# Kernel tuning notes

Hardware: AMD Instinct MI355X
Metric: run time of the kernel (lower is better)

## Reference

```python
import jax, jax.numpy as jnp
import numpy as np

B, C, P, N = 16, 512, 4, 1024


def setup_inputs() -> dict:
    key = jax.random.key(0)
    k1, k2, k3, k4, k5 = jax.random.split(key, 5)
    s = 1.0 / np.sqrt(C)
    return {
        "x": jax.random.normal(k1, (B, C, P, N), dtype=jnp.float32),
        "w_qkv": jax.random.normal(k2, (1 + 2 * C, C), dtype=jnp.float32) * s,
        "b_qkv": jax.random.normal(k3, (1 + 2 * C,), dtype=jnp.float32) * 0.01,
        "w_out": jax.random.normal(k4, (C, C), dtype=jnp.float32) * s,
        "b_out": jax.random.normal(k5, (C,), dtype=jnp.float32) * 0.01,
    }


def reference(x, w_qkv, b_qkv, w_out, b_out):
    # 1x1 conv == channel GEMM: [B,C,P,N] x [O,C] -> [B,O,P,N]
    qkv = jnp.einsum('bcpn,oc->bopn', x, w_qkv) + b_qkv[None, :, None, None]
    query = qkv[:, :1]            # [B,1,P,N]
    key_t = qkv[:, 1:1 + C]       # [B,C,P,N]
    value = qkv[:, 1 + C:]        # [B,C,P,N]
    # softmax over token axis N (attn_drop is identity at inference)
    context_scores = jax.nn.softmax(query, axis=-1)           # [B,1,P,N]
    # broadcast mul + reduce over N (fused; no explicit expand)
    context_vector = jnp.sum(key_t * context_scores, axis=-1, keepdims=True)  # [B,C,P,1]
    out = jax.nn.relu(value) * context_vector                 # [B,C,P,N]
    out = jnp.einsum('bcpn,oc->bopn', out, w_out) + b_out[None, :, None, None]
    return out
```

## Files before the change

### kernel.cpp

```cpp
#include <hip/hip_runtime.h>
#include <math.h>

#define BB 16
#define C  512
#define P  4
#define NN 1024
#define BP (BB*P)
#define PN (P*NN)

typedef short bf16x8 __attribute__((ext_vector_type(8)));
typedef float f32x4  __attribute__((ext_vector_type(4)));

__device__ __forceinline__ unsigned short bf16rne(float f) {
    unsigned u = __float_as_uint(f);
    u += 0x7FFFu + ((u >> 16) & 1u);
    return (unsigned short)(u >> 16);
}
__device__ __forceinline__ float bf16tof(unsigned short h) {
    return __uint_as_float(((unsigned)h) << 16);
}

__global__ __launch_bounds__(256) void k_split(const float* __restrict__ w_qkv,
                                               const float* __restrict__ w_out,
                                               unsigned short* __restrict__ wv_hi,
                                               unsigned short* __restrict__ wv_lo,
                                               unsigned short* __restrict__ wo_hi,
                                               unsigned short* __restrict__ wo_lo) {
    const int i = blockIdx.x * 256 + threadIdx.x;
    const int e = i * 4;
    const float* src; unsigned short *dh, *dl; int off;
    if (e < C * C) { src = w_qkv + (size_t)(1 + C) * C; dh = wv_hi; dl = wv_lo; off = e; }
    else           { src = w_out;                       dh = wo_hi; dl = wo_lo; off = e - C * C; }
    const float4 v = *reinterpret_cast<const float4*>(src + off);
    const float vv[4] = {v.x, v.y, v.z, v.w};
    unsigned short h[4], l[4];
    #pragma unroll
    for (int j = 0; j < 4; ++j) {
        h[j] = bf16rne(vv[j]);
        l[j] = bf16rne(vv[j] - bf16tof(h[j]));
    }
    uint2 ph, pl;
    ph.x = (unsigned)h[0] | ((unsigned)h[1] << 16);
    ph.y = (unsigned)h[2] | ((unsigned)h[3] << 16);
    pl.x = (unsigned)l[0] | ((unsigned)l[1] << 16);
    pl.y = (unsigned)l[2] | ((unsigned)l[3] << 16);
    *reinterpret_cast<uint2*>(dh + off) = ph;
    *reinterpret_cast<uint2*>(dl + off) = pl;
}

__global__ __launch_bounds__(256) void k_query(const float* __restrict__ x,
                                               const float* __restrict__ w_qkv,
                                               const float* __restrict__ b_qkv,
                                               float* __restrict__ query) {
    __shared__ float wq[C];
    const int bp  = blockIdx.x >> 2;
    const int q4  = blockIdx.x & 3;
    const int b   = bp >> 2, p = bp & 3;
    const int tid = threadIdx.x;
    for (int i = tid; i < C; i += 256) wq[i] = w_qkv[i];
    __syncthreads();
    const int n = q4 * 256 + tid;
    const float* xb = x + (size_t)b * C * PN + (size_t)p * NN + n;
    float a0 = 0.f, a1 = 0.f, a2 = 0.f, a3 = 0.f;
    #pragma unroll 4
    for (int c = 0; c < C; c += 4) {
        a0 = fmaf(xb[(size_t)(c + 0) * PN], wq[c + 0], a0);
        a1 = fmaf(xb[(size_t)(c + 1) * PN], wq[c + 1], a1);
        a2 = fmaf(xb[(size_t)(c + 2) * PN], wq[c + 2], a2);
        a3 = fmaf(xb[(size_t)(c + 3) * PN], wq[c + 3], a3);
    }
    query[bp * NN + n] = b_qkv[0] + ((a0 + a1) + (a2 + a3));
}

__global__ __launch_bounds__(256) void k_softmax(const float* __restrict__ query,
                                                 float* __restrict__ scores) {
    __shared__ float red[256];
    const int bp = blockIdx.x, tid = threadIdx.x;
    const float* q = query + bp * NN;
    float v[4];
    float m = -INFINITY;
    #pragma unroll
    for (int j = 0; j < 4; ++j) { v[j] = q[tid + 256 * j]; m = fmaxf(m, v[j]); }
    red[tid] = m; __syncthreads();
    for (int s = 128; s > 0; s >>= 1) {
        if (tid < s) red[tid] = fmaxf(red[tid], red[tid + s]);
        __syncthreads();
    }
    m = red[0]; __syncthreads();
    float sum = 0.f;
    #pragma unroll
    for (int j = 0; j < 4; ++j) { v[j] = expf(v[j] - m); sum += v[j]; }
    red[tid] = sum; __syncthreads();
    for (int s = 128; s > 0; s >>= 1) {
        if (tid < s) red[tid] += red[tid + s];
        __syncthreads();
    }
    const float inv = 1.0f / red[0];
    #pragma unroll
    for (int j = 0; j < 4; ++j) scores[bp * NN + tid + 256 * j] = v[j] * inv;
}

__global__ __launch_bounds__(256) void k_xs(const float* __restrict__ x,
                                            const float* __restrict__ scores,
                                            float* __restrict__ xs) {
    __shared__ float sc[NN];
    const int bp = blockIdx.x >> 3, cc = blockIdx.x & 7;
    const int b = bp >> 2, p = bp & 3;
    const int tid = threadIdx.x;
    for (int i = tid; i < NN; i += 256) sc[i] = scores[bp * NN + i];
    __syncthreads();
    const int wave = tid >> 6, lane = tid & 63;
    const float* xb = x + (size_t)b * C * PN + (size_t)p * NN;
    for (int k = 0; k < 16; ++k) {
        const int c = cc * 64 + wave * 16 + k;
        const float* row = xb + (size_t)c * PN;
        float acc = 0.f;
        #pragma unroll
        for (int j = 0; j < 16; ++j) acc = fmaf(row[lane + 64 * j], sc[lane + 64 * j], acc);
        #pragma unroll
        for (int off = 32; off > 0; off >>= 1) acc += __shfl_down(acc, off);
        if (lane == 0) xs[bp * C + c] = acc;
    }
}

__global__ __launch_bounds__(256) void k_cv(const float* __restrict__ xs,
                                            const float* __restrict__ w_qkv,
                                            const float* __restrict__ b_qkv,
                                            float* __restrict__ cv) {
    __shared__ float xsl[C];
    const int bp = blockIdx.x, tid = threadIdx.x;
    for (int i = tid; i < C; i += 256) xsl[i] = xs[bp * C + i];
    __syncthreads();
    const int wave = tid >> 6, lane = tid & 63;
    for (int o = wave; o < C; o += 4) {
        const float* wr = w_qkv + (size_t)(1 + o) * C;
        float acc = 0.f;
        #pragma unroll
        for (int j = 0; j < 8; ++j) acc = fmaf(wr[lane + 64 * j], xsl[lane + 64 * j], acc);
        #pragma unroll
        for (int off = 32; off > 0; off >>= 1) acc += __shfl_down(acc, off);
        if (lane == 0) cv[bp * C + o] = acc + b_qkv[1 + o];
    }
}

#define ALD 520
#define XLD 40
#define SLD 68

__global__ __launch_bounds__(512, 1) void k_vo(
    const float* __restrict__ x,
    const unsigned short* __restrict__ wv_hi, const unsigned short* __restrict__ wv_lo,
    const unsigned short* __restrict__ wo_hi, const unsigned short* __restrict__ wo_lo,
    const float* __restrict__ b_qkv, const float* __restrict__ b_out,
    const float* __restrict__ cv, float* __restrict__ out) {

    extern __shared__ char lds_raw[];
    unsigned short* act_hi = (unsigned short*)lds_raw;
    unsigned short* act_lo = act_hi + 64 * ALD;
    unsigned short* xt_hi  = act_lo + 64 * ALD;
    unsigned short* xt_lo  = xt_hi + 64 * XLD;
    float*          scratch = (float*)(xt_lo + 64 * XLD);

    const int nt = blockIdx.x, bp = blockIdx.y;
    const int b = bp >> 2, p = bp & 3;
    const int n0 = nt * 64;
    const int tid = threadIdx.x;
    const int w  = tid >> 6;
    const int l  = tid & 63;
    const int lr = l & 15;
    const int lg = l >> 4;

    const float* xb = x + (size_t)b * C * PN + (size_t)p * NN + n0;

    const int s_kk = tid >> 4, s_n4 = (tid & 15) * 4;
    const int g_col = tid & 63, g_k4 = (tid >> 6) * 4;

    f32x4 acc[4][4];
    #pragma unroll
    for (int m = 0; m < 4; ++m)
        #pragma unroll
        for (int n = 0; n < 4; ++n) acc[m][n] = (f32x4){0.f, 0.f, 0.f, 0.f};

    for (int kt = 0; kt < 16; ++kt) {
        *reinterpret_cast<float4*>(&scratch[s_kk * SLD + s_n4]) =
            *reinterpret_cast<const float4*>(xb + (size_t)(kt * 32 + s_kk) * PN + s_n4);
        __syncthreads();
        {
            unsigned short h[4], lo[4];
            #pragma unroll
            for (int j = 0; j < 4; ++j) {
                const float v = scratch[(g_k4 + j) * SLD + g_col];
                h[j]  = bf16rne(v);
                lo[j] = bf16rne(v - bf16tof(h[j]));
            }
            uint2 ph, pl;
            ph.x = (unsigned)h[0]  | ((unsigned)h[1]  << 16);
            ph.y = (unsigned)h[2]  | ((unsigned)h[3]  << 16);
            pl.x = (unsigned)lo[0] | ((unsigned)lo[1] << 16);
            pl.y = (unsigned)lo[2] | ((unsigned)lo[3] << 16);
            *reinterpret_cast<uint2*>(&xt_hi[g_col * XLD + g_k4]) = ph;
            *reinterpret_cast<uint2*>(&xt_lo[g_col * XLD + g_k4]) = pl;
        }
        __syncthreads();
        bf16x8 bh[4], bl[4];
        #pragma unroll
        for (int n = 0; n < 4; ++n) {
            bh[n] = *reinterpret_cast<const bf16x8*>(&xt_hi[(n * 16 + lr) * XLD + lg * 8]);
            bl[n] = *reinterpret_cast<const bf16x8*>(&xt_lo[(n * 16 + lr) * XLD + lg * 8]);
        }
        #pragma unroll
        for (int m = 0; m < 4; ++m) {
            const int row = w * 64 + m * 16 + lr;
            const bf16x8 ah = *reinterpret_cast<const bf16x8*>(&wv_hi[(size_t)row * C + kt * 32 + lg * 8]);
            const bf16x8 al = *reinterpret_cast<const bf16x8*>(&wv_lo[(size_t)row * C + kt * 32 + lg * 8]);
            #pragma unroll
            for (int n = 0; n < 4; ++n) {
                acc[m][n] = __builtin_amdgcn_mfma_f32_16x16x32_bf16(ah, bh[n], acc[m][n], 0, 0, 0);
                acc[m][n] = __builtin_amdgcn_mfma_f32_16x16x32_bf16(ah, bl[n], acc[m][n], 0, 0, 0);
                acc[m][n] = __builtin_amdgcn_mfma_f32_16x16x32_bf16(al, bh[n], acc[m][n], 0, 0, 0);
            }
        }
    }

    {
        const float* bq  = b_qkv + 1 + C;
        const float* cvb = cv + bp * C;
        #pragma unroll
        for (int m = 0; m < 4; ++m) {
            const int r0 = w * 64 + m * 16 + lg * 4;
            float bias[4], cvv[4];
            #pragma unroll
            for (int j = 0; j < 4; ++j) { bias[j] = bq[r0 + j]; cvv[j] = cvb[r0 + j]; }
            #pragma unroll
            for (int n = 0; n < 4; ++n) {
                unsigned short hh[4], ll[4];
                #pragma unroll
                for (int j = 0; j < 4; ++j) {
                    const float av = fmaxf(acc[m][n][j] + bias[j], 0.f) * cvv[j];
                    hh[j] = bf16rne(av);
                    ll[j] = bf16rne(av - bf16tof(hh[j]));
                }
                uint2 ph, pl;
                ph.x = (unsigned)hh[0] | ((unsigned)hh[1] << 16);
                ph.y = (unsigned)hh[2] | ((unsigned)hh[3] << 16);
                pl.x = (unsigned)ll[0] | ((unsigned)ll[1] << 16);
                pl.y = (unsigned)ll[2] | ((unsigned)ll[3] << 16);
                *reinterpret_cast<uint2*>(&act_hi[(n * 16 + lr) * ALD + r0]) = ph;
                *reinterpret_cast<uint2*>(&act_lo[(n * 16 + lr) * ALD + r0]) = pl;
            }
        }
    }
    __syncthreads();

    f32x4 acc2[4][4];
    #pragma unroll
    for (int m = 0; m < 4; ++m)
        #pragma unroll
        for (int n = 0; n < 4; ++n) acc2[m][n] = (f32x4){0.f, 0.f, 0.f, 0.f};

    for (int kt = 0; kt < 16; ++kt) {
        bf16x8 bh[4], bl[4];
        #pragma unroll
        for (int n = 0; n < 4; ++n) {
            bh[n] = *reinterpret_cast<const bf16x8*>(&act_hi[(n * 16 + lr) * ALD + kt * 32 + lg * 8]);
            bl[n] = *reinterpret_cast<const bf16x8*>(&act_lo[(n * 16 + lr) * ALD + kt * 32 + lg * 8]);
        }
        #pragma unroll
        for (int m = 0; m < 4; ++m) {
            const int row = w * 64 + m * 16 + lr;
            const bf16x8 ah = *reinterpret_cast<const bf16x8*>(&wo_hi[(size_t)row * C + kt * 32 + lg * 8]);
            const bf16x8 al = *reinterpret_cast<const bf16x8*>(&wo_lo[(size_t)row * C + kt * 32 + lg * 8]);
            #pragma unroll
            for (int n = 0; n < 4; ++n) {
                acc2[m][n] = __builtin_amdgcn_mfma_f32_16x16x32_bf16(ah, bh[n], acc2[m][n], 0, 0, 0);
                acc2[m][n] = __builtin_amdgcn_mfma_f32_16x16x32_bf16(ah, bl[n], acc2[m][n], 0, 0, 0);
                acc2[m][n] = __builtin_amdgcn_mfma_f32_16x16x32_bf16(al, bh[n], acc2[m][n], 0, 0, 0);
            }
        }
    }

    #pragma unroll
    for (int m = 0; m < 4; ++m) {
        #pragma unroll
        for (int j = 0; j < 4; ++j) {
            const int row = w * 64 + m * 16 + lg * 4 + j;
            const float bo = b_out[row];
            float* orow = out + ((size_t)(b * C + row) * P + p) * NN + n0;
            #pragma unroll
            for (int n = 0; n < 4; ++n)
                orow[n * 16 + lr] = acc2[m][n][j] + bo;
        }
    }
}

extern "C" void kernel_launch(void* const* d_in, const int* in_sizes, int n_in,
                              void* d_out, int out_size, void* d_ws, size_t ws_size,
                              hipStream_t stream) {
    const float* x     = (const float*)d_in[0];
    const float* w_qkv = (const float*)d_in[1];
    const float* b_qkv = (const float*)d_in[2];
    const float* w_out = (const float*)d_in[3];
    const float* b_out = (const float*)d_in[4];
    float* out = (float*)d_out;

    float* query  = (float*)d_ws;
    float* scores = query + BP * NN;
    float* xs     = scores + BP * NN;
    float* cv     = xs + BP * C;
    unsigned short* wsp = (unsigned short*)(cv + BP * C);
    unsigned short* wv_hi = wsp;
    unsigned short* wv_lo = wsp + C * C;
    unsigned short* wo_hi = wsp + 2 * C * C;
    unsigned short* wo_lo = wsp + 3 * C * C;

    k_split  <<<dim3(512),    256, 0, stream>>>(w_qkv, w_out, wv_hi, wv_lo, wo_hi, wo_lo);
    k_query  <<<dim3(BP * 4), 256, 0, stream>>>(x, w_qkv, b_qkv, query);
    k_softmax<<<dim3(BP),     256, 0, stream>>>(query, scores);
    k_xs     <<<dim3(BP * 8), 256, 0, stream>>>(x, scores, xs);
    k_cv     <<<dim3(BP),     256, 0, stream>>>(xs, w_qkv, b_qkv, cv);

    const size_t ldsbytes = (size_t)(2 * 64 * ALD + 2 * 64 * XLD) * 2 + (size_t)(32 * SLD) * 4;
    k_vo<<<dim3(16, BP), 512, ldsbytes, stream>>>(x, wv_hi, wv_lo, wo_hi, wo_lo,
                                                  b_qkv, b_out, cv, out);
}
```

Measured before the change: 649.1 us.

## Double-buffer x tiles in k_vo with fragment-ordered LDS, and vectorize the reductions

k_vo now prefetches the next x k-slice into registers while MFMAs run on the current one. It converts the slice straight into a double-buffered LDS layout that matches the MFMA fragment order, which removes the fp32 scratch transpose and one barrier per iteration. The intermediate activation is also stored in fragment order, so it can be read back with contiguous 16-byte loads. k_query is split over channel chunks with float4 loads, writing partial sums that k_softmax adds up. The bias is dropped there, which is valid because softmax is shift-invariant. k_xs uses float4 loads across more blocks. The trade-offs are an extra partial-sum buffer and higher register pressure from the prefetch.

```diff
diff --git a/kernel.cpp b/kernel.cpp
--- a/kernel.cpp
+++ b/kernel.cpp
@@ -10,30 +10,31 @@
 
 typedef short bf16x8 __attribute__((ext_vector_type(8)));
 typedef float f32x4  __attribute__((ext_vector_type(4)));
-
-__device__ __forceinline__ unsigned short bf16rne(float f) {
+typedef unsigned short ushort_t;
+
+__device__ __forceinline__ ushort_t bf16rne(float f) {
     unsigned u = __float_as_uint(f);
     u += 0x7FFFu + ((u >> 16) & 1u);
-    return (unsigned short)(u >> 16);
-}
-__device__ __forceinline__ float bf16tof(unsigned short h) {
+    return (ushort_t)(u >> 16);
+}
+__device__ __forceinline__ float bf16tof(ushort_t h) {
     return __uint_as_float(((unsigned)h) << 16);
 }
 
 __global__ __launch_bounds__(256) void k_split(const float* __restrict__ w_qkv,
                                                const float* __restrict__ w_out,
-                                               unsigned short* __restrict__ wv_hi,
-                                               unsigned short* __restrict__ wv_lo,
-                                               unsigned short* __restrict__ wo_hi,
-                                               unsigned short* __restrict__ wo_lo) {
+                                               ushort_t* __restrict__ wv_hi,
+                                               ushort_t* __restrict__ wv_lo,
+                                               ushort_t* __restrict__ wo_hi,
+                                               ushort_t* __restrict__ wo_lo) {
     const int i = blockIdx.x * 256 + threadIdx.x;
     const int e = i * 4;
-    const float* src; unsigned short *dh, *dl; int off;
+    const float* src; ushort_t *dh, *dl; int off;
     if (e < C * C) { src = w_qkv + (size_t)(1 + C) * C; dh = wv_hi; dl = wv_lo; off = e; }
     else           { src = w_out;                       dh = wo_hi; dl = wo_lo; off = e - C * C; }
     const float4 v = *reinterpret_cast<const float4*>(src + off);
     const float vv[4] = {v.x, v.y, v.z, v.w};
-    unsigned short h[4], l[4];
+    ushort_t h[4], l[4];
     #pragma unroll
     for (int j = 0; j < 4; ++j) {
         h[j] = bf16rne(vv[j]);
@@ -50,37 +51,42 @@
 
 __global__ __launch_bounds__(256) void k_query(const float* __restrict__ x,
                                                const float* __restrict__ w_qkv,
-                                               const float* __restrict__ b_qkv,
-                                               float* __restrict__ query) {
-    __shared__ float wq[C];
-    const int bp  = blockIdx.x >> 2;
-    const int q4  = blockIdx.x & 3;
-    const int b   = bp >> 2, p = bp & 3;
+                                               float4* __restrict__ qpart4) {
+    __shared__ float wq[64];
+    const int bp = blockIdx.x >> 3, cc = blockIdx.x & 7;
+    const int b = bp >> 2, p = bp & 3;
     const int tid = threadIdx.x;
-    for (int i = tid; i < C; i += 256) wq[i] = w_qkv[i];
-    __syncthreads();
-    const int n = q4 * 256 + tid;
-    const float* xb = x + (size_t)b * C * PN + (size_t)p * NN + n;
-    float a0 = 0.f, a1 = 0.f, a2 = 0.f, a3 = 0.f;
-    #pragma unroll 4
-    for (int c = 0; c < C; c += 4) {
-        a0 = fmaf(xb[(size_t)(c + 0) * PN], wq[c + 0], a0);
-        a1 = fmaf(xb[(size_t)(c + 1) * PN], wq[c + 1], a1);
-        a2 = fmaf(xb[(size_t)(c + 2) * PN], wq[c + 2], a2);
-        a3 = fmaf(xb[(size_t)(c + 3) * PN], wq[c + 3], a3);
-    }
-    query[bp * NN + n] = b_qkv[0] + ((a0 + a1) + (a2 + a3));
-}
-
-__global__ __launch_bounds__(256) void k_softmax(const float* __restrict__ query,
-                                                 float* __restrict__ scores) {
+    if (tid < 64) wq[tid] = w_qkv[cc * 64 + tid];
+    __syncthreads();
+    const float* xb = x + (size_t)b * C * PN + (size_t)p * NN;
+    f32x4 acc[8];
+    #pragma unroll
+    for (int a = 0; a < 8; ++a) acc[a] = (f32x4){0.f, 0.f, 0.f, 0.f};
+    #pragma unroll 8
+    for (int i = 0; i < 64; ++i) {
+        const float4 v = *reinterpret_cast<const float4*>(xb + (size_t)(cc * 64 + i) * PN + tid * 4);
+        const float wv = wq[i];
+        acc[i & 7][0] = fmaf(v.x, wv, acc[i & 7][0]);
+        acc[i & 7][1] = fmaf(v.y, wv, acc[i & 7][1]);
+        acc[i & 7][2] = fmaf(v.z, wv, acc[i & 7][2]);
+        acc[i & 7][3] = fmaf(v.w, wv, acc[i & 7][3]);
+    }
+    f32x4 s = ((acc[0] + acc[1]) + (acc[2] + acc[3])) + ((acc[4] + acc[5]) + (acc[6] + acc[7]));
+    float4 o; o.x = s[0]; o.y = s[1]; o.z = s[2]; o.w = s[3];
+    qpart4[(cc * BP + bp) * 256 + tid] = o;
+}
+
+__global__ __launch_bounds__(256) void k_softmax(const float4* __restrict__ qpart4,
+                                                 float4* __restrict__ scores4) {
     __shared__ float red[256];
     const int bp = blockIdx.x, tid = threadIdx.x;
-    const float* q = query + bp * NN;
-    float v[4];
-    float m = -INFINITY;
-    #pragma unroll
-    for (int j = 0; j < 4; ++j) { v[j] = q[tid + 256 * j]; m = fmaxf(m, v[j]); }
+    float v[4] = {0.f, 0.f, 0.f, 0.f};
+    #pragma unroll
+    for (int cc = 0; cc < 8; ++cc) {
+        const float4 q = qpart4[(cc * BP + bp) * 256 + tid];
+        v[0] += q.x; v[1] += q.y; v[2] += q.z; v[3] += q.w;
+    }
+    float m = fmaxf(fmaxf(v[0], v[1]), fmaxf(v[2], v[3]));
     red[tid] = m; __syncthreads();
     for (int s = 128; s > 0; s >>= 1) {
         if (tid < s) red[tid] = fmaxf(red[tid], red[tid + s]);
@@ -96,27 +102,36 @@
         __syncthreads();
     }
     const float inv = 1.0f / red[0];
-    #pragma unroll
-    for (int j = 0; j < 4; ++j) scores[bp * NN + tid + 256 * j] = v[j] * inv;
+    float4 o; o.x = v[0] * inv; o.y = v[1] * inv; o.z = v[2] * inv; o.w = v[3] * inv;
+    scores4[bp * 256 + tid] = o;
 }
 
 __global__ __launch_bounds__(256) void k_xs(const float* __restrict__ x,
-                                            const float* __restrict__ scores,
+                                            const float4* __restrict__ scores4,
                                             float* __restrict__ xs) {
-    __shared__ float sc[NN];
-    const int bp = blockIdx.x >> 3, cc = blockIdx.x & 7;
+    __shared__ float4 sc4[256];
+    const int bp = blockIdx.x >> 4, cc = blockIdx.x & 15;
     const int b = bp >> 2, p = bp & 3;
     const int tid = threadIdx.x;
-    for (int i = tid; i < NN; i += 256) sc[i] = scores[bp * NN + i];
+    sc4[tid] = scores4[bp * 256 + tid];
     __syncthreads();
     const int wave = tid >> 6, lane = tid & 63;
     const float* xb = x + (size_t)b * C * PN + (size_t)p * NN;
-    for (int k = 0; k < 16; ++k) {
-        const int c = cc * 64 + wave * 16 + k;
-        const float* row = xb + (size_t)c * PN;
-        float acc = 0.f;
-        #pragma unroll
-        for (int j = 0; j < 16; ++j) acc = fmaf(row[lane + 64 * j], sc[lane + 64 * j], acc);
+    #pragma unroll
+    for (int r = 0; r < 8; ++r) {
+        const int c = cc * 32 + wave * 8 + r;
+        const float4* row4 = reinterpret_cast<const float4*>(xb + (size_t)c * PN);
+        float a0 = 0.f, a1 = 0.f, a2 = 0.f, a3 = 0.f;
+        #pragma unroll
+        for (int j = 0; j < 4; ++j) {
+            const float4 xv = row4[lane + 64 * j];
+            const float4 sv = sc4[lane + 64 * j];
+            a0 = fmaf(xv.x, sv.x, a0);
+            a1 = fmaf(xv.y, sv.y, a1);
+            a2 = fmaf(xv.z, sv.z, a2);
+            a3 = fmaf(xv.w, sv.w, a3);
+        }
+        float acc = (a0 + a1) + (a2 + a3);
         #pragma unroll
         for (int off = 32; off > 0; off >>= 1) acc += __shfl_down(acc, off);
         if (lane == 0) xs[bp * C + c] = acc;
@@ -143,23 +158,19 @@
     }
 }
 
-#define ALD 520
-#define XLD 40
-#define SLD 68
+#define XTFH 2048
 
 __global__ __launch_bounds__(512, 1) void k_vo(
     const float* __restrict__ x,
-    const unsigned short* __restrict__ wv_hi, const unsigned short* __restrict__ wv_lo,
-    const unsigned short* __restrict__ wo_hi, const unsigned short* __restrict__ wo_lo,
+    const ushort_t* __restrict__ wv_hi, const ushort_t* __restrict__ wv_lo,
+    const ushort_t* __restrict__ wo_hi, const ushort_t* __restrict__ wo_lo,
     const float* __restrict__ b_qkv, const float* __restrict__ b_out,
     const float* __restrict__ cv, float* __restrict__ out) {
 
     extern __shared__ char lds_raw[];
-    unsigned short* act_hi = (unsigned short*)lds_raw;
-    unsigned short* act_lo = act_hi + 64 * ALD;
-    unsigned short* xt_hi  = act_lo + 64 * ALD;
-    unsigned short* xt_lo  = xt_hi + 64 * XLD;
-    float*          scratch = (float*)(xt_lo + 64 * XLD);
+    ushort_t* actf_hi = (ushort_t*)lds_raw;
+    ushort_t* actf_lo = actf_hi + 16 * 4 * 64 * 8;
+    ushort_t* xtf     = actf_lo + 16 * 4 * 64 * 8;
 
     const int nt = blockIdx.x, bp = blockIdx.y;
     const int b = bp >> 2, p = bp & 3;
@@ -172,8 +183,9 @@
 
     const float* xb = x + (size_t)b * C * PN + (size_t)p * NN + n0;
 
-    const int s_kk = tid >> 4, s_n4 = (tid & 15) * 4;
-    const int g_col = tid & 63, g_k4 = (tid >> 6) * 4;
+    const int g_col = tid & 63;
+    const int g_k4  = (tid >> 6) * 4;
+    const int st_off = (((g_col >> 4) * 64 + (g_k4 >> 3) * 16 + (g_col & 15)) * 8) + (g_k4 & 7);
 
     f32x4 acc[4][4];
     #pragma unroll
@@ -181,45 +193,71 @@
         #pragma unroll
         for (int n = 0; n < 4; ++n) acc[m][n] = (f32x4){0.f, 0.f, 0.f, 0.f};
 
+    {
+        float xg[4];
+        #pragma unroll
+        for (int jj = 0; jj < 4; ++jj) xg[jj] = xb[(size_t)(g_k4 + jj) * PN + g_col];
+        ushort_t h[4], lo[4];
+        #pragma unroll
+        for (int jj = 0; jj < 4; ++jj) {
+            h[jj]  = bf16rne(xg[jj]);
+            lo[jj] = bf16rne(xg[jj] - bf16tof(h[jj]));
+        }
+        uint2 ph, pl;
+        ph.x = (unsigned)h[0]  | ((unsigned)h[1]  << 16);
+        ph.y = (unsigned)h[2]  | ((unsigned)h[3]  << 16);
+        pl.x = (unsigned)lo[0] | ((unsigned)lo[1] << 16);
+        pl.y = (unsigned)lo[2] | ((unsigned)lo[3] << 16);
+        *reinterpret_cast<uint2*>(&xtf[st_off])        = ph;
+        *reinterpret_cast<uint2*>(&xtf[XTFH + st_off]) = pl;
+    }
+    __syncthreads();
+
     for (int kt = 0; kt < 16; ++kt) {
-        *reinterpret_cast<float4*>(&scratch[s_kk * SLD + s_n4]) =
-            *reinterpret_cast<const float4*>(xb + (size_t)(kt * 32 + s_kk) * PN + s_n4);
-        __syncthreads();
-        {
-            unsigned short h[4], lo[4];
-            #pragma unroll
-            for (int j = 0; j < 4; ++j) {
-                const float v = scratch[(g_k4 + j) * SLD + g_col];
-                h[j]  = bf16rne(v);
-                lo[j] = bf16rne(v - bf16tof(h[j]));
+        const int cur = kt & 1;
+        float xg[4];
+        if (kt < 15) {
+            #pragma unroll
+            for (int jj = 0; jj < 4; ++jj)
+                xg[jj] = xb[(size_t)((kt + 1) * 32 + g_k4 + jj) * PN + g_col];
+        }
+        const ushort_t* xh = xtf + cur * 2 * XTFH;
+        const ushort_t* xl = xh + XTFH;
+        bf16x8 bh[4], bl[4];
+        #pragma unroll
+        for (int n = 0; n < 4; ++n) {
+            bh[n] = *reinterpret_cast<const bf16x8*>(&xh[(n * 64 + l) * 8]);
+            bl[n] = *reinterpret_cast<const bf16x8*>(&xl[(n * 64 + l) * 8]);
+        }
+        #pragma unroll
+        for (int m = 0; m < 4; ++m) {
+            const int row = w * 64 + m * 16 + lr;
+            const bf16x8 ah = *reinterpret_cast<const bf16x8*>(&wv_hi[(size_t)row * C + kt * 32 + lg * 8]);
+            const bf16x8 al = *reinterpret_cast<const bf16x8*>(&wv_lo[(size_t)row * C + kt * 32 + lg * 8]);
+            #pragma unroll
+            for (int n = 0; n < 4; ++n) {
+                acc[m][n] = __builtin_amdgcn_mfma_f32_16x16x32_bf16(ah, bh[n], acc[m][n], 0, 0, 0);
+                acc[m][n] = __builtin_amdgcn_mfma_f32_16x16x32_bf16(ah, bl[n], acc[m][n], 0, 0, 0);
+                acc[m][n] = __builtin_amdgcn_mfma_f32_16x16x32_bf16(al, bh[n], acc[m][n], 0, 0, 0);
+            }
+        }
+        if (kt < 15) {
+            ushort_t* dh = xtf + (cur ^ 1) * 2 * XTFH;
+            ushort_t h[4], lo[4];
+            #pragma unroll
+            for (int jj = 0; jj < 4; ++jj) {
+                h[jj]  = bf16rne(xg[jj]);
+                lo[jj] = bf16rne(xg[jj] - bf16tof(h[jj]));
             }
             uint2 ph, pl;
             ph.x = (unsigned)h[0]  | ((unsigned)h[1]  << 16);
             ph.y = (unsigned)h[2]  | ((unsigned)h[3]  << 16);
             pl.x = (unsigned)lo[0] | ((unsigned)lo[1] << 16);
             pl.y = (unsigned)lo[2] | ((unsigned)lo[3] << 16);
-            *reinterpret_cast<uint2*>(&xt_hi[g_col * XLD + g_k4]) = ph;
-            *reinterpret_cast<uint2*>(&xt_lo[g_col * XLD + g_k4]) = pl;
+            *reinterpret_cast<uint2*>(&dh[st_off])        = ph;
+            *reinterpret_cast<uint2*>(&dh[XTFH + st_off]) = pl;
         }
         __syncthreads();
-        bf16x8 bh[4], bl[4];
-        #pragma unroll
-        for (int n = 0; n < 4; ++n) {
-            bh[n] = *reinterpret_cast<const bf16x8*>(&xt_hi[(n * 16 + lr) * XLD + lg * 8]);
-            bl[n] = *reinterpret_cast<const bf16x8*>(&xt_lo[(n * 16 + lr) * XLD + lg * 8]);
-        }
-        #pragma unroll
-        for (int m = 0; m < 4; ++m) {
-            const int row = w * 64 + m * 16 + lr;
-            const bf16x8 ah = *reinterpret_cast<const bf16x8*>(&wv_hi[(size_t)row * C + kt * 32 + lg * 8]);
-            const bf16x8 al = *reinterpret_cast<const bf16x8*>(&wv_lo[(size_t)row * C + kt * 32 + lg * 8]);
-            #pragma unroll
-            for (int n = 0; n < 4; ++n) {
-                acc[m][n] = __builtin_amdgcn_mfma_f32_16x16x32_bf16(ah, bh[n], acc[m][n], 0, 0, 0);
-                acc[m][n] = __builtin_amdgcn_mfma_f32_16x16x32_bf16(ah, bl[n], acc[m][n], 0, 0, 0);
-                acc[m][n] = __builtin_amdgcn_mfma_f32_16x16x32_bf16(al, bh[n], acc[m][n], 0, 0, 0);
-            }
-        }
     }
 
     {
@@ -227,13 +265,16 @@
         const float* cvb = cv + bp * C;
         #pragma unroll
         for (int m = 0; m < 4; ++m) {
-            const int r0 = w * 64 + m * 16 + lg * 4;
+            const int rbase = w * 64 + m * 16 + lg * 4;
+            const int ktp = w * 2 + (m >> 1);
+            const int lgp = (m * 2 + (lg >> 1)) & 3;
+            const int j0p = (lg & 1) * 4;
             float bias[4], cvv[4];
             #pragma unroll
-            for (int j = 0; j < 4; ++j) { bias[j] = bq[r0 + j]; cvv[j] = cvb[r0 + j]; }
+            for (int j = 0; j < 4; ++j) { bias[j] = bq[rbase + j]; cvv[j] = cvb[rbase + j]; }
             #pragma unroll
             for (int n = 0; n < 4; ++n) {
-                unsigned short hh[4], ll[4];
+                ushort_t hh[4], ll[4];
                 #pragma unroll
                 for (int j = 0; j < 4; ++j) {
                     const float av = fmaxf(acc[m][n][j] + bias[j], 0.f) * cvv[j];
@@ -245,8 +286,9 @@
                 ph.y = (unsigned)hh[2] | ((unsigned)hh[3] << 16);
                 pl.x = (unsigned)ll[0] | ((unsigned)ll[1] << 16);
                 pl.y = (unsigned)ll[2] | ((unsigned)ll[3] << 16);
-                *reinterpret_cast<uint2*>(&act_hi[(n * 16 + lr) * ALD + r0]) = ph;
-                *reinterpret_cast<uint2*>(&act_lo[(n * 16 + lr) * ALD + r0]) = pl;
+                const int off = ((ktp * 4 + n) * 64 + lgp * 16 + lr) * 8 + j0p;
+                *reinterpret_cast<uint2*>(&actf_hi[off]) = ph;
+                *reinterpret_cast<uint2*>(&actf_lo[off]) = pl;
             }
         }
     }
@@ -262,8 +304,8 @@
         bf16x8 bh[4], bl[4];
         #pragma unroll
         for (int n = 0; n < 4; ++n) {
-            bh[n] = *reinterpret_cast<const bf16x8*>(&act_hi[(n * 16 + lr) * ALD + kt * 32 + lg * 8]);
-            bl[n] = *reinterpret_cast<const bf16x8*>(&act_lo[(n * 16 + lr) * ALD + kt * 32 + lg * 8]);
+            bh[n] = *reinterpret_cast<const bf16x8*>(&actf_hi[((kt * 4 + n) * 64 + l) * 8]);
+            bl[n] = *reinterpret_cast<const bf16x8*>(&actf_lo[((kt * 4 + n) * 64 + l) * 8]);
         }
         #pragma unroll
         for (int m = 0; m < 4; ++m) {
@@ -303,23 +345,23 @@
     const float* b_out = (const float*)d_in[4];
     float* out = (float*)d_out;
 
-    float* query  = (float*)d_ws;
-    float* scores = query + BP * NN;
+    float* qpart  = (float*)d_ws;
+    float* scores = qpart + 8 * BP * NN;
     float* xs     = scores + BP * NN;
     float* cv     = xs + BP * C;
-    unsigned short* wsp = (unsigned short*)(cv + BP * C);
-    unsigned short* wv_hi = wsp;
-    unsigned short* wv_lo = wsp + C * C;
-    unsigned short* wo_hi = wsp + 2 * C * C;
-    unsigned short* wo_lo = wsp + 3 * C * C;
-
-    k_split  <<<dim3(512),    256, 0, stream>>>(w_qkv, w_out, wv_hi, wv_lo, wo_hi, wo_lo);
-    k_query  <<<dim3(BP * 4), 256, 0, stream>>>(x, w_qkv, b_qkv, query);
-    k_softmax<<<dim3(BP),     256, 0, stream>>>(query, scores);
-    k_xs     <<<dim3(BP * 8), 256, 0, stream>>>(x, scores, xs);
-    k_cv     <<<dim3(BP),     256, 0, stream>>>(xs, w_qkv, b_qkv, cv);
-
-    const size_t ldsbytes = (size_t)(2 * 64 * ALD + 2 * 64 * XLD) * 2 + (size_t)(32 * SLD) * 4;
+    ushort_t* wsp = (ushort_t*)(cv + BP * C);
+    ushort_t* wv_hi = wsp;
+    ushort_t* wv_lo = wsp + C * C;
+    ushort_t* wo_hi = wsp + 2 * C * C;
+    ushort_t* wo_lo = wsp + 3 * C * C;
+
+    k_split  <<<dim3(512),     256, 0, stream>>>(w_qkv, w_out, wv_hi, wv_lo, wo_hi, wo_lo);
+    k_query  <<<dim3(BP * 8),  256, 0, stream>>>(x, w_qkv, (float4*)qpart);
+    k_softmax<<<dim3(BP),      256, 0, stream>>>((const float4*)qpart, (float4*)scores);
+    k_xs     <<<dim3(BP * 16), 256, 0, stream>>>(x, (const float4*)scores, xs);
+    k_cv     <<<dim3(BP),      256, 0, stream>>>(xs, w_qkv, b_qkv, cv);
+
+    const size_t ldsbytes = (size_t)(2 * 16 * 4 * 64 * 8 + 2 * 2 * XTFH) * sizeof(ushort_t);
     k_vo<<<dim3(16, BP), 512, ldsbytes, stream>>>(x, wv_hi, wv_lo, wo_hi, wo_lo,
                                                   b_qkv, b_out, cv, out);
 }
```

New measurement: 624.5 us. 1.04x faster.
